# Performance work log

Hardware: AMD Instinct MI355X
Metric: run time of the kernel (lower is better)

## Reference

```python
import jax, jax.numpy as jnp
import numpy as np

DIM, HEADS, PAIR_DIM = 256, 8, 128
B, S, N = 1, 128, 256
DH = DIM // HEADS
SCALE = DH ** -0.5
EPS = 1e-5


def setup_inputs() -> dict:
    key = jax.random.key(0)
    ks = jax.random.split(key, 12)
    s = lambda fan_in: 1.0 / np.sqrt(fan_in)
    return {
        "msa": jax.random.normal(ks[0], (B, S, N, DIM), jnp.float32),
        "pair": jax.random.normal(ks[1], (B, N, N, PAIR_DIM), jnp.float32),
        "mask": jax.random.randint(ks[2], (B, N, N), 0, 2, jnp.int32),
        "Wqkv": jax.random.normal(ks[3], (3 * DIM, DIM), jnp.float32) * s(DIM),
        "bqkv": jnp.zeros((3 * DIM,), jnp.float32),
        "Wout": jax.random.normal(ks[4], (DIM, DIM), jnp.float32) * s(DIM),
        "bout": jnp.zeros((DIM,), jnp.float32),
        "Wpb": jax.random.normal(ks[5], (HEADS, PAIR_DIM), jnp.float32) * s(PAIR_DIM),
        "bpb": jnp.zeros((HEADS,), jnp.float32),
        "gamma": jnp.ones((DIM,), jnp.float32),
        "beta": jnp.zeros((DIM,), jnp.float32),
    }


def reference(msa, pair, mask, Wqkv, bqkv, Wout, bout, Wpb, bpb, gamma, beta):
    # qkv projection: [B,S,N,3*DIM] -> [B,S,N,3,H,DH]
    qkv = (msa @ Wqkv.T + bqkv).reshape(B, S, N, 3, HEADS, DH)
    q, k, v = qkv[..., 0, :, :], qkv[..., 1, :, :], qkv[..., 2, :, :]
    # scores [B,S,H,N,N]
    attn = jnp.einsum('bsnhc,bsmhc->bshnm', q, k) * SCALE
    attn = jnp.where(mask[:, None, None, :, :] == 0, -1e9, attn)
    # pair bias: [B,N,N,P] -> [B,1,H,N,N]
    pair_bias = (pair @ Wpb.T + bpb).transpose(0, 3, 1, 2)[:, None]
    attn = jax.nn.softmax(attn + pair_bias, axis=-1)
    out = jnp.einsum('bshnm,bsmhc->bsnhc', attn, v).reshape(B, S, N, DIM)
    out = out @ Wout.T + bout
    # residual + layernorm
    x = msa + out
    mu = jnp.mean(x, axis=-1, keepdims=True)
    var = jnp.var(x, axis=-1, keepdims=True)
    return (x - mu) * jax.lax.rsqrt(var + EPS) * gamma + beta
```

## Files before the change

kernel.cpp:

```cpp
#include <hip/hip_runtime.h>
#include <cstdint>
#include <cstddef>

typedef unsigned short u16;
typedef __bf16 bf16x8 __attribute__((ext_vector_type(8)));
typedef float f32x4 __attribute__((ext_vector_type(4)));
typedef unsigned int u32x4 __attribute__((ext_vector_type(4)));

#define SCALE_QK 0.17677669529663687f

__device__ __forceinline__ u16 f2bf(float f){ return __builtin_bit_cast(u16, (__bf16)f); }
__device__ __forceinline__ float bf2f(u16 u){ unsigned v = ((unsigned)u)<<16; return __builtin_bit_cast(float, v); }
__device__ __forceinline__ bf16x8 ldfrag_g(const u16* p){
  return __builtin_bit_cast(bf16x8, *reinterpret_cast<const u32x4*>(p));
}
__device__ __forceinline__ void gload16(const u16* g, u16* lds){
  __builtin_amdgcn_global_load_lds((const __attribute__((address_space(1))) unsigned int*)g,
                                   (__attribute__((address_space(3))) unsigned int*)lds, 16, 0, 0);
}

__global__ __launch_bounds__(256) void k_cvt(const float* __restrict__ src,
                                             u16* __restrict__ dst, int n4){
  int stride = gridDim.x * blockDim.x;
  for (int idx = blockIdx.x*blockDim.x + threadIdx.x; idx < n4; idx += stride){
    float4 v = reinterpret_cast<const float4*>(src)[idx];
    ushort4 o;
    o.x = f2bf(v.x); o.y = f2bf(v.y); o.z = f2bf(v.z); o.w = f2bf(v.w);
    reinterpret_cast<ushort4*>(dst)[idx] = o;
  }
}

__global__ __launch_bounds__(256) void k_cvt2(const float* __restrict__ a, u16* __restrict__ da,
                                              const float* __restrict__ b, u16* __restrict__ db){
  int bid = blockIdx.x;
  if (bid < 192){
    int idx = bid*256 + threadIdx.x;
    float4 v = reinterpret_cast<const float4*>(a)[idx];
    ushort4 o; o.x=f2bf(v.x); o.y=f2bf(v.y); o.z=f2bf(v.z); o.w=f2bf(v.w);
    reinterpret_cast<ushort4*>(da)[idx] = o;
  } else {
    int idx = (bid-192)*256 + threadIdx.x;
    float4 v = reinterpret_cast<const float4*>(b)[idx];
    ushort4 o; o.x=f2bf(v.x); o.y=f2bf(v.y); o.z=f2bf(v.z); o.w=f2bf(v.w);
    reinterpret_cast<ushort4*>(db)[idx] = o;
  }
}

__global__ __launch_bounds__(256) void k_pair_bias(const float* __restrict__ pair,
        const int* __restrict__ mask, const float* __restrict__ Wpb,
        const float* __restrict__ bpb, u16* __restrict__ bT){
  __shared__ float wsm[8][128];
  __shared__ float bsm[8];
  int tid = threadIdx.x;
  for (int i = tid; i < 1024; i += 256) wsm[i>>7][i&127] = Wpb[i];
  if (tid < 8) bsm[tid] = bpb[tid];
  __syncthreads();
  int g = tid>>4, l = tid&15;
  int row = blockIdx.x*16 + g;
  const float4* p = reinterpret_cast<const float4*>(pair + (size_t)row*128);
  float4 a0 = p[l];
  float4 a1 = p[l+16];
  int c0 = 4*l, c1 = 64 + 4*l;
  float acc[8];
#pragma unroll
  for (int hh=0; hh<8; hh++){
    acc[hh] = a0.x*wsm[hh][c0] + a0.y*wsm[hh][c0+1] + a0.z*wsm[hh][c0+2] + a0.w*wsm[hh][c0+3]
            + a1.x*wsm[hh][c1] + a1.y*wsm[hh][c1+1] + a1.z*wsm[hh][c1+2] + a1.w*wsm[hh][c1+3];
  }
#pragma unroll
  for (int hh=0; hh<8; hh++){
    float v = acc[hh];
    v += __shfl_xor(v,1); v += __shfl_xor(v,2); v += __shfl_xor(v,4); v += __shfl_xor(v,8);
    acc[hh] = v;
  }
  if (l == 0){
    float mb = (mask[row] == 0) ? -1e9f : 0.0f;
    int n = row>>8, m = row&255;
#pragma unroll
    for (int hh=0; hh<8; hh++)
      bT[hh*65536 + m*256 + n] = f2bf(acc[hh] + bsm[hh] + mb);
  }
}

__global__ __launch_bounds__(256, 3) void k_qkv(const u16* __restrict__ A,
                                                const u16* __restrict__ B,
                                                const float* __restrict__ bq,
                                                u16* __restrict__ qkv){
  __shared__ __align__(16) u16 Al[128*64];
  __shared__ __align__(16) u16 Bl[128*64];
  const int tid = threadIdx.x;
  const int w = tid>>6, l = tid&63;
  const int wm = w>>1, wn = w&1;
  const int m0 = blockIdx.y*128, n0 = blockIdx.x*128;
  const int lr = l&15, lg = l>>4;
  f32x4 acc[4][4] = {};
  for (int kt=0; kt<4; ++kt){
    const int k0 = kt*64;
    __syncthreads();
#pragma unroll
    for (int j=0;j<4;j++){
      int ch = w*256 + j*64 + l;
      int r = ch>>3, sl = ch&7;
      gload16(A + (size_t)(m0+r)*256 + k0 + ((sl^(r&7))*8), Al + (size_t)(w*256 + j*64)*8);
      gload16(B + (size_t)(n0+r)*256 + k0 + ((sl^(r&7))*8), Bl + (size_t)(w*256 + j*64)*8);
    }
    __syncthreads();
#pragma unroll
    for (int ks=0; ks<2; ++ks){
      bf16x8 af[4], bfr[4];
#pragma unroll
      for (int t=0;t<4;t++){
        int ra = wm*64 + t*16 + lr;
        int sa = (ks*4 + lg) ^ (ra&7);
        af[t] = __builtin_bit_cast(bf16x8, *reinterpret_cast<const u32x4*>(&Al[ra*64 + sa*8]));
        int rb = wn*64 + t*16 + lr;
        int sb = (ks*4 + lg) ^ (rb&7);
        bfr[t] = __builtin_bit_cast(bf16x8, *reinterpret_cast<const u32x4*>(&Bl[rb*64 + sb*8]));
      }
#pragma unroll
      for (int tm=0;tm<4;tm++)
#pragma unroll
        for (int tn=0;tn<4;tn++)
          acc[tm][tn] = __builtin_amdgcn_mfma_f32_16x16x32_bf16(af[tm], bfr[tn], acc[tm][tn], 0,0,0);
    }
  }
#pragma unroll
  for (int tn=0;tn<4;tn++){
    int c = n0 + wn*64 + tn*16 + lr;
    int t3 = c>>8, hh = (c>>5)&7, dh = c&31;
    float bb = bq[c];
    u16* obase = qkv + (size_t)(t3*8+hh)*32768*32 + dh;
#pragma unroll
    for (int tm=0;tm<4;tm++){
#pragma unroll
      for (int rr=0;rr<4;rr++){
        int m = m0 + wm*64 + tm*16 + lg*4 + rr;
        obase[(size_t)m*32] = f2bf(acc[tm][tn][rr] + bb);
      }
    }
  }
}

__global__ __launch_bounds__(256, 3) void k_attn(const u16* __restrict__ qkv,
                                                 const u16* __restrict__ bT,
                                                 u16* __restrict__ O){
  __shared__ __align__(16) u16 vT[32*256];
  __shared__ __align__(16) u16 P[4][32*64];
  const int h = blockIdx.x, s = blockIdx.y, z = blockIdx.z;
  const int tid = threadIdx.x;
  const int w = tid>>6, l = tid&63;
  const int lr = l&15, lg = l>>4;
  const int n0 = z*128 + 32*w;
  const u16* qb = qkv + ((size_t)h*32768 + s*256)*32;
  const u16* kb = qkv + ((size_t)(8+h)*32768 + s*256)*32;
  const u16* vb = qkv + ((size_t)(16+h)*32768 + s*256)*32;
  const u16* bb = bT + h*65536;

#pragma unroll
  for (int i=0;i<4;i++){
    int flat4 = tid + 256*i;
    int m = flat4>>2, d0 = (flat4&3)*8;
    u32x4 d = *reinterpret_cast<const u32x4*>(vb + (size_t)m*32 + d0);
    u16 tmp[8];
    *reinterpret_cast<u32x4*>(tmp) = d;
#pragma unroll
    for (int j=0;j<8;j++){
      int dh = d0 + j;
      vT[dh*256 + (((m>>3)^(dh&7))*8) + (m&7)] = tmp[j];
    }
  }
  __syncthreads();

  bf16x8 qf[2];
#pragma unroll
  for (int t=0;t<2;t++)
    qf[t] = ldfrag_g(qb + (size_t)(n0 + t*16 + lr)*32 + lg*8);

  f32x4 oacc[2][2] = {};
  float mrun[2][4], lrun[2][4];
#pragma unroll
  for (int t=0;t<2;t++)
#pragma unroll
    for (int rr=0;rr<4;rr++){ mrun[t][rr] = -3e38f; lrun[t][rr] = 0.f; }

  for (int mt=0; mt<4; ++mt){
    ushort4 b4[2][4];
#pragma unroll
    for (int t=0;t<2;t++)
#pragma unroll
      for (int tn=0;tn<4;tn++)
        b4[t][tn] = *reinterpret_cast<const ushort4*>(
            bb + (size_t)(mt*64 + tn*16 + lr)*256 + n0 + t*16 + lg*4);
    bf16x8 kf[4];
#pragma unroll
    for (int tn=0;tn<4;tn++)
      kf[tn] = ldfrag_g(kb + (size_t)(mt*64 + tn*16 + lr)*32 + lg*8);
    f32x4 sacc[2][4] = {};
#pragma unroll
    for (int t=0;t<2;t++)
#pragma unroll
      for (int tn=0;tn<4;tn++)
        sacc[t][tn] = __builtin_amdgcn_mfma_f32_16x16x32_bf16(qf[t], kf[tn], sacc[t][tn], 0,0,0);
#pragma unroll
    for (int t=0;t<2;t++)
#pragma unroll
      for (int tn=0;tn<4;tn++){
        float bc[4] = { bf2f(b4[t][tn].x), bf2f(b4[t][tn].y), bf2f(b4[t][tn].z), bf2f(b4[t][tn].w) };
#pragma unroll
        for (int rr=0;rr<4;rr++)
          sacc[t][tn][rr] = sacc[t][tn][rr]*SCALE_QK + bc[rr];
      }
#pragma unroll
    for (int t=0;t<2;t++){
#pragma unroll
      for (int rr=0;rr<4;rr++){
        float mx = fmaxf(fmaxf(sacc[t][0][rr], sacc[t][1][rr]),
                         fmaxf(sacc[t][2][rr], sacc[t][3][rr]));
        mx = fmaxf(mx, __shfl_xor(mx,1));
        mx = fmaxf(mx, __shfl_xor(mx,2));
        mx = fmaxf(mx, __shfl_xor(mx,4));
        mx = fmaxf(mx, __shfl_xor(mx,8));
        float mo = mrun[t][rr];
        float mn = fmaxf(mo, mx);
        float corr = __expf(mo - mn);
        mrun[t][rr] = mn;
        float ps = 0.f;
#pragma unroll
        for (int tn=0;tn<4;tn++){
          float p = __expf(sacc[t][tn][rr] - mn);
          sacc[t][tn][rr] = p;
          ps += p;
        }
        ps += __shfl_xor(ps,1);
        ps += __shfl_xor(ps,2);
        ps += __shfl_xor(ps,4);
        ps += __shfl_xor(ps,8);
        lrun[t][rr] = lrun[t][rr]*corr + ps;
        oacc[t][0][rr] *= corr;
        oacc[t][1][rr] *= corr;
      }
    }
#pragma unroll
    for (int t=0;t<2;t++){
#pragma unroll
      for (int rr=0;rr<4;rr++){
        int row = t*16 + lg*4 + rr;
        int rb = row*64;
        int sx = row&7;
#pragma unroll
        for (int tn=0;tn<4;tn++){
          int col = tn*16 + lr;
          P[w][rb + (((col>>3)^sx)*8) + (col&7)] = f2bf(sacc[t][tn][rr]);
        }
      }
    }
#pragma unroll
    for (int kk=0;kk<2;kk++){
      bf16x8 vf[2];
#pragma unroll
      for (int dt=0;dt<2;dt++){
        int c = dt*16 + lr;
        int slot = (mt*8 + kk*4 + lg) ^ (c&7);
        vf[dt] = __builtin_bit_cast(bf16x8, *reinterpret_cast<const u32x4*>(&vT[c*256 + slot*8]));
      }
#pragma unroll
      for (int t=0;t<2;t++){
        int ra = t*16 + lr;
        int sa = (kk*4 + lg) ^ (ra&7);
        bf16x8 pf = __builtin_bit_cast(bf16x8, *reinterpret_cast<const u32x4*>(&P[w][ra*64 + sa*8]));
        oacc[t][0] = __builtin_amdgcn_mfma_f32_16x16x32_bf16(pf, vf[0], oacc[t][0], 0,0,0);
        oacc[t][1] = __builtin_amdgcn_mfma_f32_16x16x32_bf16(pf, vf[1], oacc[t][1], 0,0,0);
      }
    }
  }
#pragma unroll
  for (int t=0;t<2;t++){
#pragma unroll
    for (int rr=0;rr<4;rr++){
      int n = n0 + t*16 + lg*4 + rr;
      float inv = 1.0f / lrun[t][rr];
      size_t rowb = (size_t)(s*256 + n)*256 + h*32;
#pragma unroll
      for (int dt=0;dt<2;dt++)
        O[rowb + dt*16 + lr] = f2bf(oacc[t][dt][rr]*inv);
    }
  }
}

__global__ __launch_bounds__(256, 3) void k_out_ln(const u16* __restrict__ A,
        const u16* __restrict__ Wo, const float* __restrict__ bo,
        const float* __restrict__ msa, const float* __restrict__ gamma,
        const float* __restrict__ beta, float* __restrict__ out){
  __shared__ __align__(16) u16 Al[64*64];
  __shared__ __align__(16) u16 Wl[256*64];
  __shared__ float redS[64][4];
  __shared__ float redQ[64][4];
  const int tid = threadIdx.x;
  const int w = tid>>6, l = tid&63;
  const int lr = l&15, lg = l>>4;
  const int m0 = blockIdx.x*64;
  f32x4 acc[4][4] = {};
  for (int kt=0;kt<4;kt++){
    const int k0 = kt*64;
    __syncthreads();
#pragma unroll
    for (int j=0;j<2;j++){
      int ch = w*128 + j*64 + l;
      int r = ch>>3, sl = ch&7;
      gload16(A + (size_t)(m0+r)*256 + k0 + ((sl^(r&7))*8), Al + (size_t)(w*128 + j*64)*8);
    }
#pragma unroll
    for (int j=0;j<8;j++){
      int ch = w*512 + j*64 + l;
      int r = ch>>3, sl = ch&7;
      gload16(Wo + (size_t)r*256 + k0 + ((sl^(r&7))*8), Wl + (size_t)(w*512 + j*64)*8);
    }
    __syncthreads();
#pragma unroll
    for (int ks=0;ks<2;ks++){
      bf16x8 af[4], bfr[4];
#pragma unroll
      for (int t=0;t<4;t++){
        int ra = t*16 + lr;
        int sa = (ks*4+lg) ^ (ra&7);
        af[t] = __builtin_bit_cast(bf16x8, *reinterpret_cast<const u32x4*>(&Al[ra*64 + sa*8]));
        int rb = w*64 + t*16 + lr;
        int sb = (ks*4+lg) ^ (rb&7);
        bfr[t] = __builtin_bit_cast(bf16x8, *reinterpret_cast<const u32x4*>(&Wl[rb*64 + sb*8]));
      }
#pragma unroll
      for (int tm=0;tm<4;tm++)
#pragma unroll
        for (int tn=0;tn<4;tn++)
          acc[tm][tn] = __builtin_amdgcn_mfma_f32_16x16x32_bf16(af[tm], bfr[tn], acc[tm][tn], 0,0,0);
    }
  }
#pragma unroll
  for (int tn=0;tn<4;tn++){
    int c = w*64 + tn*16 + lr;
    float bc = bo[c];
#pragma unroll
    for (int tm=0;tm<4;tm++)
#pragma unroll
      for (int rr=0;rr<4;rr++){
        int m = m0 + tm*16 + lg*4 + rr;
        acc[tm][tn][rr] += bc + msa[(size_t)m*256 + c];
      }
  }
#pragma unroll
  for (int tm=0;tm<4;tm++){
#pragma unroll
    for (int rr=0;rr<4;rr++){
      float sS = 0.f, sQ = 0.f;
#pragma unroll
      for (int tn=0;tn<4;tn++){
        float v = acc[tm][tn][rr];
        sS += v; sQ += v*v;
      }
      sS += __shfl_xor(sS,1); sS += __shfl_xor(sS,2); sS += __shfl_xor(sS,4); sS += __shfl_xor(sS,8);
      sQ += __shfl_xor(sQ,1); sQ += __shfl_xor(sQ,2); sQ += __shfl_xor(sQ,4); sQ += __shfl_xor(sQ,8);
      if (lr == 0){
        int row = tm*16 + lg*4 + rr;
        redS[row][w] = sS;
        redQ[row][w] = sQ;
      }
    }
  }
  __syncthreads();
#pragma unroll
  for (int tm=0;tm<4;tm++){
#pragma unroll
    for (int rr=0;rr<4;rr++){
      int row = tm*16 + lg*4 + rr;
      float S = redS[row][0]+redS[row][1]+redS[row][2]+redS[row][3];
      float Q = redQ[row][0]+redQ[row][1]+redQ[row][2]+redQ[row][3];
      float mu = S * (1.0f/256.0f);
      float var = Q * (1.0f/256.0f) - mu*mu;
      float inv = rsqrtf(var + 1e-5f);
      int m = m0 + row;
#pragma unroll
      for (int tn=0;tn<4;tn++){
        int c = w*64 + tn*16 + lr;
        out[(size_t)m*256 + c] = (acc[tm][tn][rr]-mu)*inv*gamma[c] + beta[c];
      }
    }
  }
}

extern "C" void kernel_launch(void* const* d_in, const int* in_sizes, int n_in,
                              void* d_out, int out_size, void* d_ws, size_t ws_size,
                              hipStream_t stream) {
  const float* msa  = (const float*)d_in[0];
  const float* pair = (const float*)d_in[1];
  const int*   mask = (const int*)d_in[2];
  const float* Wqkv = (const float*)d_in[3];
  const float* bqkv = (const float*)d_in[4];
  const float* Wout = (const float*)d_in[5];
  const float* bout = (const float*)d_in[6];
  const float* Wpb  = (const float*)d_in[7];
  const float* bpb  = (const float*)d_in[8];
  const float* gamma= (const float*)d_in[9];
  const float* beta = (const float*)d_in[10];
  float* out = (float*)d_out;

  char* ws = (char*)d_ws;
  u16*   msa_bf  = (u16*)(ws);
  u16*   wqkv_bf = (u16*)(ws + 16777216);
  u16*   wout_bf = (u16*)(ws + 17170432);
  u16*   biasT   = (u16*)(ws + 17301504);
  u16*   qkvb    = (u16*)(ws + 18350080);
  u16*   Ob      = (u16*)(ws + 68681728);

  k_cvt<<<4096, 256, 0, stream>>>(msa, msa_bf, 8388608/4);
  k_cvt2<<<256, 256, 0, stream>>>(Wqkv, wqkv_bf, Wout, wout_bf);
  k_pair_bias<<<4096, 256, 0, stream>>>(pair, mask, Wpb, bpb, biasT);
  k_qkv<<<dim3(6,256), 256, 0, stream>>>(msa_bf, wqkv_bf, bqkv, qkvb);
  k_attn<<<dim3(8,128,2), 256, 0, stream>>>(qkvb, biasT, Ob);
  k_out_ln<<<512, 256, 0, stream>>>(Ob, wout_bf, bout, msa, gamma, beta, out);
}
```

Before: 248.2 us.

## Replace online softmax with full-row two-pass softmax using exp2 and prescaled bias

The attention kernel now computes all 256 key scores per row in registers, takes one max and one sum, and drops the running-max correction rescales of the online softmax. The pair bias is prescaled by 1/ln2 and the QK scale folded with log2e so the exponential uses the native exp2 instruction. The extra register pressure is accommodated by lowering launch bounds occupancy from 3 to 2 blocks per CU, which risks fewer waves for latency hiding.

After: 233.4 us. 6.0% less time.

```diff
diff --git a/kernel.cpp b/kernel.cpp
--- a/kernel.cpp
+++ b/kernel.cpp
@@ -7,7 +7,8 @@
 typedef float f32x4 __attribute__((ext_vector_type(4)));
 typedef unsigned int u32x4 __attribute__((ext_vector_type(4)));
 
-#define SCALE_QK 0.17677669529663687f
+#define SCALE_QK_LOG2 0.25509904f
+#define INV_LN2 1.4426950408889634f
 
 __device__ __forceinline__ u16 f2bf(float f){ return __builtin_bit_cast(u16, (__bf16)f); }
 __device__ __forceinline__ float bf2f(u16 u){ unsigned v = ((unsigned)u)<<16; return __builtin_bit_cast(float, v); }
@@ -78,7 +79,7 @@
     int n = row>>8, m = row&255;
 #pragma unroll
     for (int hh=0; hh<8; hh++)
-      bT[hh*65536 + m*256 + n] = f2bf(acc[hh] + bsm[hh] + mb);
+      bT[hh*65536 + m*256 + n] = f2bf((acc[hh] + bsm[hh] + mb) * INV_LN2);
   }
 }
 
@@ -141,7 +142,7 @@
   }
 }
 
-__global__ __launch_bounds__(256, 3) void k_attn(const u16* __restrict__ qkv,
+__global__ __launch_bounds__(256, 2) void k_attn(const u16* __restrict__ qkv,
                                                  const u16* __restrict__ bT,
                                                  u16* __restrict__ O){
   __shared__ __align__(16) u16 vT[32*256];
@@ -176,70 +177,65 @@
   for (int t=0;t<2;t++)
     qf[t] = ldfrag_g(qb + (size_t)(n0 + t*16 + lr)*32 + lg*8);
 
+  f32x4 sacc[2][16] = {};
+#pragma unroll
+  for (int kt=0; kt<4; ++kt){
+    bf16x8 kf[4];
+#pragma unroll
+    for (int tn=0;tn<4;tn++)
+      kf[tn] = ldfrag_g(kb + (size_t)(kt*64 + tn*16 + lr)*32 + lg*8);
+#pragma unroll
+    for (int t=0;t<2;t++)
+#pragma unroll
+      for (int tn=0;tn<4;tn++)
+        sacc[t][kt*4+tn] = __builtin_amdgcn_mfma_f32_16x16x32_bf16(qf[t], kf[tn], sacc[t][kt*4+tn], 0,0,0);
+  }
+
+#pragma unroll
+  for (int kt=0;kt<4;kt++){
+#pragma unroll
+    for (int t=0;t<2;t++)
+#pragma unroll
+      for (int tn=0;tn<4;tn++){
+        ushort4 b4 = *reinterpret_cast<const ushort4*>(
+            bb + (size_t)(kt*64 + tn*16 + lr)*256 + n0 + t*16 + lg*4);
+        float bc[4] = { bf2f(b4.x), bf2f(b4.y), bf2f(b4.z), bf2f(b4.w) };
+#pragma unroll
+        for (int rr=0;rr<4;rr++)
+          sacc[t][kt*4+tn][rr] = sacc[t][kt*4+tn][rr]*SCALE_QK_LOG2 + bc[rr];
+      }
+  }
+
+  float inv_l[2][4];
+#pragma unroll
+  for (int t=0;t<2;t++){
+#pragma unroll
+    for (int rr=0;rr<4;rr++){
+      float mx = sacc[t][0][rr];
+#pragma unroll
+      for (int j=1;j<16;j++) mx = fmaxf(mx, sacc[t][j][rr]);
+      mx = fmaxf(mx, __shfl_xor(mx,1));
+      mx = fmaxf(mx, __shfl_xor(mx,2));
+      mx = fmaxf(mx, __shfl_xor(mx,4));
+      mx = fmaxf(mx, __shfl_xor(mx,8));
+      float ps = 0.f;
+#pragma unroll
+      for (int j=0;j<16;j++){
+        float p = __builtin_amdgcn_exp2f(sacc[t][j][rr] - mx);
+        sacc[t][j][rr] = p;
+        ps += p;
+      }
+      ps += __shfl_xor(ps,1);
+      ps += __shfl_xor(ps,2);
+      ps += __shfl_xor(ps,4);
+      ps += __shfl_xor(ps,8);
+      inv_l[t][rr] = 1.0f / ps;
+    }
+  }
+
   f32x4 oacc[2][2] = {};
-  float mrun[2][4], lrun[2][4];
-#pragma unroll
-  for (int t=0;t<2;t++)
-#pragma unroll
-    for (int rr=0;rr<4;rr++){ mrun[t][rr] = -3e38f; lrun[t][rr] = 0.f; }
-
+#pragma unroll
   for (int mt=0; mt<4; ++mt){
-    ushort4 b4[2][4];
-#pragma unroll
-    for (int t=0;t<2;t++)
-#pragma unroll
-      for (int tn=0;tn<4;tn++)
-        b4[t][tn] = *reinterpret_cast<const ushort4*>(
-            bb + (size_t)(mt*64 + tn*16 + lr)*256 + n0 + t*16 + lg*4);
-    bf16x8 kf[4];
-#pragma unroll
-    for (int tn=0;tn<4;tn++)
-      kf[tn] = ldfrag_g(kb + (size_t)(mt*64 + tn*16 + lr)*32 + lg*8);
-    f32x4 sacc[2][4] = {};
-#pragma unroll
-    for (int t=0;t<2;t++)
-#pragma unroll
-      for (int tn=0;tn<4;tn++)
-        sacc[t][tn] = __builtin_amdgcn_mfma_f32_16x16x32_bf16(qf[t], kf[tn], sacc[t][tn], 0,0,0);
-#pragma unroll
-    for (int t=0;t<2;t++)
-#pragma unroll
-      for (int tn=0;tn<4;tn++){
-        float bc[4] = { bf2f(b4[t][tn].x), bf2f(b4[t][tn].y), bf2f(b4[t][tn].z), bf2f(b4[t][tn].w) };
-#pragma unroll
-        for (int rr=0;rr<4;rr++)
-          sacc[t][tn][rr] = sacc[t][tn][rr]*SCALE_QK + bc[rr];
-      }
-#pragma unroll
-    for (int t=0;t<2;t++){
-#pragma unroll
-      for (int rr=0;rr<4;rr++){
-        float mx = fmaxf(fmaxf(sacc[t][0][rr], sacc[t][1][rr]),
-                         fmaxf(sacc[t][2][rr], sacc[t][3][rr]));
-        mx = fmaxf(mx, __shfl_xor(mx,1));
-        mx = fmaxf(mx, __shfl_xor(mx,2));
-        mx = fmaxf(mx, __shfl_xor(mx,4));
-        mx = fmaxf(mx, __shfl_xor(mx,8));
-        float mo = mrun[t][rr];
-        float mn = fmaxf(mo, mx);
-        float corr = __expf(mo - mn);
-        mrun[t][rr] = mn;
-        float ps = 0.f;
-#pragma unroll
-        for (int tn=0;tn<4;tn++){
-          float p = __expf(sacc[t][tn][rr] - mn);
-          sacc[t][tn][rr] = p;
-          ps += p;
-        }
-        ps += __shfl_xor(ps,1);
-        ps += __shfl_xor(ps,2);
-        ps += __shfl_xor(ps,4);
-        ps += __shfl_xor(ps,8);
-        lrun[t][rr] = lrun[t][rr]*corr + ps;
-        oacc[t][0][rr] *= corr;
-        oacc[t][1][rr] *= corr;
-      }
-    }
 #pragma unroll
     for (int t=0;t<2;t++){
 #pragma unroll
@@ -250,7 +246,7 @@
 #pragma unroll
         for (int tn=0;tn<4;tn++){
           int col = tn*16 + lr;
-          P[w][rb + (((col>>3)^sx)*8) + (col&7)] = f2bf(sacc[t][tn][rr]);
+          P[w][rb + (((col>>3)^sx)*8) + (col&7)] = f2bf(sacc[t][mt*4+tn][rr]);
         }
       }
     }
@@ -278,7 +274,7 @@
 #pragma unroll
     for (int rr=0;rr<4;rr++){
       int n = n0 + t*16 + lg*4 + rr;
-      float inv = 1.0f / lrun[t][rr];
+      float inv = inv_l[t][rr];
       size_t rowb = (size_t)(s*256 + n)*256 + h*32;
 #pragma unroll
       for (int dt=0;dt<2;dt++)
```
